# Optimization experiments

Measured on AMD Instinct MI355X. Metric: run time of the kernel, lower is better.

## Reference

```python
import jax, jax.numpy as jnp
import numpy as np

S = 14            # grid size, hardcoded via torch.arange(14) in the original
N = S * S         # 196 cells (one box per cell in this implementation)
B = 1024
NUM_CLS = 90
LAMBDA_COORD = 5.0
LAMBDA_NOOBJ = 0.5


def setup_inputs() -> dict:
    key = jax.random.key(0)
    k1, k2, k3 = jax.random.split(key, 3)
    p_yolo = jax.random.uniform(k1, (B, S, S, 5 + NUM_CLS), dtype=jnp.float32)
    g_yolo = jax.random.uniform(k2, (B, S, S, 5 + NUM_CLS), dtype=jnp.float32)
    obj = jax.random.uniform(k3, (B, S, S)) < 0.05
    g_yolo = g_yolo.at[..., 4].set(jnp.where(obj, g_yolo[..., 4], 0.0))
    return {"p_yolo": p_yolo, "g_yolo": g_yolo}


def reference(p_yolo, g_yolo):
    Bc = p_yolo.shape[0]
    dt = p_yolo.dtype
    # which cells contain an object (coo_mask), flattened row-major like torch
    valid = (g_yolo[..., 4] > 0).reshape(Bc, N)          # [B, N] bool
    vf = valid.astype(dt)
    pred = p_yolo[..., :5].reshape(Bc, N, 5)             # [B, N, 5]
    targ = g_yolo[..., :5].reshape(Bc, N, 5)             # [B, N, 5]

    # grid cell coordinates (row-major flatten matches torch boolean-mask order)
    rows = jnp.repeat(jnp.arange(S, dtype=dt), S)        # [N]
    cols = jnp.tile(jnp.arange(S, dtype=dt), S)          # [N]
    # cal_iou converts target xy to global coords IN PLACE before the xy mse
    tx = cols / S + targ[..., 0] / S                     # [B, N]
    ty = rows / S + targ[..., 1] / S
    tw, th = targ[..., 2], targ[..., 3]

    # IoU [B, Npred, Ntarg] -- same math as cal_iou (pred stays in local coords)
    dx = jnp.abs(tx[:, None, :] - pred[:, :, None, 0])
    dy = jnp.abs(ty[:, None, :] - pred[:, :, None, 1])
    sw = (tw[:, None, :] + pred[:, :, None, 2]) * 0.5
    sh = (th[:, None, :] + pred[:, :, None, 3]) * 0.5
    inter = jnp.maximum((sw - dx) * (sh - dy), 0.0)      # clamp after product, as original
    union = (tw * th)[:, None, :] + (pred[..., 2] * pred[..., 3])[:, :, None] - inter
    iou = inter / union

    # per-target best prediction (max over pred dim = dim 0 in original)
    best_iou = iou.max(axis=1)                           # [B, N]
    best_idx = iou.argmax(axis=1)                        # [B, N] int
    bp = jnp.take_along_axis(pred, best_idx[..., None], axis=1)  # [B, N, 5]

    # localization (xy) loss: matched pred xy vs global target xy, sum over valid targets
    xy_loss = jnp.sum(vf * ((bp[..., 0] - tx) ** 2 + (bp[..., 1] - ty) ** 2))

    # confidence loss for matched boxes: (pred_conf * iou - 1)^2
    con_obj_loss = jnp.sum(vf * (bp[..., 4] * best_iou - 1.0) ** 2)

    # no-object confidence loss: preds NOT selected by any valid target,
    # only counted for images that contain at least one object (original skips empty images)
    hit = jnp.zeros((Bc, N), dtype=dt).at[jnp.arange(Bc)[:, None], best_idx].max(vf)
    has_obj = vf.max(axis=1)                             # [B]
    nocon_obj_loss = jnp.sum(has_obj[:, None] * (1.0 - hit) * pred[..., 4] ** 2)

    # class loss over object cells (batched over all images)
    cls_d = (p_yolo[..., 5:] - g_yolo[..., 5:]).reshape(Bc, N, NUM_CLS)
    con_class_loss = jnp.sum(vf[..., None] * cls_d ** 2)

    # NOTE: original total doubles xy_loss and never uses wh_loss -- kept faithful
    total = (LAMBDA_COORD * (xy_loss + xy_loss) + con_obj_loss
             + LAMBDA_NOOBJ * nocon_obj_loss + con_class_loss) / Bc
    return total
```

## Files before the change

kernel.cpp:

```cpp
#include <hip/hip_runtime.h>
#include <math.h>

#define GS 14
#define NCELL 196
#define NCLS 90
#define CH 95

__global__ __launch_bounds__(256) void yolo_loss_main(
    const float* __restrict__ p, const float* __restrict__ g,
    float* __restrict__ ws, int B)
{
    int b = blockIdx.x;
    if (b >= B) return;
    const float* pb = p + (size_t)b * NCELL * CH;
    const float* gb = g + (size_t)b * NCELL * CH;

    __shared__ float sp[NCELL][5];
    __shared__ float st[NCELL][5];
    __shared__ int   svalid[NCELL];
    __shared__ int   scount;
    __shared__ int   shit[NCELL];
    __shared__ float sred[4];

    const int tid  = threadIdx.x;
    const int wave = tid >> 6;
    const int lane = tid & 63;

    for (int i = tid; i < NCELL * 5; i += 256) {
        int c = i / 5, j = i - c * 5;
        sp[c][j] = pb[c * CH + j];
        st[c][j] = gb[c * CH + j];
    }
    for (int i = tid; i < NCELL; i += 256) shit[i] = 0;
    __syncthreads();

    if (tid == 0) {
        int cnt = 0;
        for (int c = 0; c < NCELL; ++c)
            if (st[c][4] > 0.0f) svalid[cnt++] = c;
        scount = cnt;
    }
    __syncthreads();
    const int count = scount;

    float xy_acc = 0.0f, con_acc = 0.0f;

    for (int vt = wave; vt < count; vt += 4) {
        const int t = svalid[vt];
        const float tx = __fadd_rn(__fdiv_rn((float)(t % GS), (float)GS),
                                   __fdiv_rn(st[t][0], (float)GS));
        const float ty = __fadd_rn(__fdiv_rn((float)(t / GS), (float)GS),
                                   __fdiv_rn(st[t][1], (float)GS));
        const float tw = st[t][2], th = st[t][3];
        const float twth = __fmul_rn(tw, th);

        float bi = -INFINITY;
        int   bidx = 0x7fffffff;
        for (int pp = lane; pp < NCELL; pp += 64) {
            const float px = sp[pp][0], py = sp[pp][1];
            const float pw = sp[pp][2], ph = sp[pp][3];
            const float dx = fabsf(__fsub_rn(tx, px));
            const float dy = fabsf(__fsub_rn(ty, py));
            const float sw = __fmul_rn(__fadd_rn(tw, pw), 0.5f);
            const float sh = __fmul_rn(__fadd_rn(th, ph), 0.5f);
            const float inter = fmaxf(__fmul_rn(__fsub_rn(sw, dx),
                                                __fsub_rn(sh, dy)), 0.0f);
            const float uni = __fsub_rn(__fadd_rn(twth, __fmul_rn(pw, ph)), inter);
            const float iou = __fdiv_rn(inter, uni);
            if (iou > bi || (iou == bi && pp < bidx)) { bi = iou; bidx = pp; }
        }
        for (int off = 32; off; off >>= 1) {
            const float oi  = __shfl_xor(bi, off);
            const int   oid = __shfl_xor(bidx, off);
            if (oi > bi || (oi == bi && oid < bidx)) { bi = oi; bidx = oid; }
        }
        if (lane == 0) {
            const float d0 = __fsub_rn(sp[bidx][0], tx);
            const float d1 = __fsub_rn(sp[bidx][1], ty);
            xy_acc += __fadd_rn(__fmul_rn(d0, d0), __fmul_rn(d1, d1));
            const float cc = __fsub_rn(__fmul_rn(sp[bidx][4], bi), 1.0f);
            con_acc += __fmul_rn(cc, cc);
            shit[bidx] = 1;
        }
    }
    __syncthreads();

    float nocon_acc = 0.0f;
    if (count > 0) {
        for (int pp = tid; pp < NCELL; pp += 256) {
            if (!shit[pp]) {
                const float c = sp[pp][4];
                nocon_acc += c * c;
            }
        }
    }

    float cls_acc = 0.0f;
    const int totalc = count * NCLS;
    for (int i = tid; i < totalc; i += 256) {
        const int vt = i / NCLS, j = i - vt * NCLS;
        const int t = svalid[vt];
        const float d = pb[t * CH + 5 + j] - gb[t * CH + 5 + j];
        cls_acc += d * d;
    }

    float tot = 10.0f * xy_acc + con_acc + 0.5f * nocon_acc + cls_acc;
    for (int off = 32; off; off >>= 1) tot += __shfl_xor(tot, off);
    if (lane == 0) sred[wave] = tot;
    __syncthreads();
    if (tid == 0) ws[b] = sred[0] + sred[1] + sred[2] + sred[3];
}

__global__ __launch_bounds__(256) void yolo_loss_reduce(
    const float* __restrict__ ws, float* __restrict__ out, int B)
{
    const int tid = threadIdx.x;
    float s = 0.0f;
    for (int i = tid; i < B; i += 256) s += ws[i];
    for (int off = 32; off; off >>= 1) s += __shfl_xor(s, off);
    __shared__ float sr[4];
    if ((tid & 63) == 0) sr[tid >> 6] = s;
    __syncthreads();
    if (tid == 0) out[0] = (sr[0] + sr[1] + sr[2] + sr[3]) / (float)B;
}

extern "C" void kernel_launch(void* const* d_in, const int* in_sizes, int n_in,
                              void* d_out, int out_size, void* d_ws, size_t ws_size,
                              hipStream_t stream) {
    const float* p = (const float*)d_in[0];
    const float* g = (const float*)d_in[1];
    float* out = (float*)d_out;
    float* ws  = (float*)d_ws;
    const int B = in_sizes[0] / (NCELL * CH);

    yolo_loss_main<<<B, 256, 0, stream>>>(p, g, ws, B);
    yolo_loss_reduce<<<1, 256, 0, stream>>>(ws, out, B);
}
```

Measured before the change: 36.41 us.

## Fuse per-image loss and final reduction via atomicAdd; ballot-based valid-cell compaction

Replaces the serial single-thread scan that built the valid-target list with a wave ballot plus popcount prefix, so each of the 196 cells is checked and compacted in parallel. The head loads become one thread per cell. The separate reduction kernel is removed: each block atomically adds its scaled partial sum to the output, which is zeroed by a memset beforehand. This cuts one kernel launch and a serial bottleneck, but makes the float summation order nondeterministic.

```diff
diff --git a/kernel.cpp b/kernel.cpp
--- a/kernel.cpp
+++ b/kernel.cpp
@@ -6,19 +6,18 @@
 #define NCLS 90
 #define CH 95
 
-__global__ __launch_bounds__(256) void yolo_loss_main(
+__global__ __launch_bounds__(256) void yolo_loss_fused(
     const float* __restrict__ p, const float* __restrict__ g,
-    float* __restrict__ ws, int B)
+    float* __restrict__ out, float inv_b)
 {
-    int b = blockIdx.x;
-    if (b >= B) return;
+    const int b = blockIdx.x;
     const float* pb = p + (size_t)b * NCELL * CH;
     const float* gb = g + (size_t)b * NCELL * CH;
 
     __shared__ float sp[NCELL][5];
     __shared__ float st[NCELL][5];
     __shared__ int   svalid[NCELL];
-    __shared__ int   scount;
+    __shared__ unsigned long long smask[4];
     __shared__ int   shit[NCELL];
     __shared__ float sred[4];
 
@@ -26,22 +25,32 @@
     const int wave = tid >> 6;
     const int lane = tid & 63;
 
-    for (int i = tid; i < NCELL * 5; i += 256) {
-        int c = i / 5, j = i - c * 5;
-        sp[c][j] = pb[c * CH + j];
-        st[c][j] = gb[c * CH + j];
+    bool v = false;
+    if (tid < NCELL) {
+        const float* pr = pb + tid * CH;
+        const float* gr = gb + tid * CH;
+        float g4 = gr[4];
+        #pragma unroll
+        for (int j = 0; j < 4; ++j) { sp[tid][j] = pr[j]; st[tid][j] = gr[j]; }
+        sp[tid][4] = pr[4];
+        st[tid][4] = g4;
+        shit[tid] = 0;
+        v = g4 > 0.0f;
     }
-    for (int i = tid; i < NCELL; i += 256) shit[i] = 0;
+    const unsigned long long m = __ballot(v);
+    if (lane == 0) smask[wave] = m;
     __syncthreads();
 
-    if (tid == 0) {
-        int cnt = 0;
-        for (int c = 0; c < NCELL; ++c)
-            if (st[c][4] > 0.0f) svalid[cnt++] = c;
-        scount = cnt;
+    int base = 0;
+    #pragma unroll
+    for (int w = 0; w < 4; ++w) if (w < wave) base += __popcll(smask[w]);
+    const int count = __popcll(smask[0]) + __popcll(smask[1]) +
+                      __popcll(smask[2]) + __popcll(smask[3]);
+    if (v) {
+        const int pos = base + __popcll(m & ((1ull << lane) - 1ull));
+        svalid[pos] = tid;
     }
     __syncthreads();
-    const int count = scount;
 
     float xy_acc = 0.0f, con_acc = 0.0f;
 
@@ -86,12 +95,10 @@
     __syncthreads();
 
     float nocon_acc = 0.0f;
-    if (count > 0) {
-        for (int pp = tid; pp < NCELL; pp += 256) {
-            if (!shit[pp]) {
-                const float c = sp[pp][4];
-                nocon_acc += c * c;
-            }
+    if (count > 0 && tid < NCELL) {
+        if (!shit[tid]) {
+            const float c = sp[tid][4];
+            nocon_acc = c * c;
         }
     }
 
@@ -108,20 +115,10 @@
     for (int off = 32; off; off >>= 1) tot += __shfl_xor(tot, off);
     if (lane == 0) sred[wave] = tot;
     __syncthreads();
-    if (tid == 0) ws[b] = sred[0] + sred[1] + sred[2] + sred[3];
-}
-
-__global__ __launch_bounds__(256) void yolo_loss_reduce(
-    const float* __restrict__ ws, float* __restrict__ out, int B)
-{
-    const int tid = threadIdx.x;
-    float s = 0.0f;
-    for (int i = tid; i < B; i += 256) s += ws[i];
-    for (int off = 32; off; off >>= 1) s += __shfl_xor(s, off);
-    __shared__ float sr[4];
-    if ((tid & 63) == 0) sr[tid >> 6] = s;
-    __syncthreads();
-    if (tid == 0) out[0] = (sr[0] + sr[1] + sr[2] + sr[3]) / (float)B;
+    if (tid == 0) {
+        const float bl = sred[0] + sred[1] + sred[2] + sred[3];
+        atomicAdd(out, bl * inv_b);
+    }
 }
 
 extern "C" void kernel_launch(void* const* d_in, const int* in_sizes, int n_in,
@@ -130,9 +127,8 @@
     const float* p = (const float*)d_in[0];
     const float* g = (const float*)d_in[1];
     float* out = (float*)d_out;
-    float* ws  = (float*)d_ws;
     const int B = in_sizes[0] / (NCELL * CH);
 
-    yolo_loss_main<<<B, 256, 0, stream>>>(p, g, ws, B);
-    yolo_loss_reduce<<<1, 256, 0, stream>>>(ws, out, B);
+    hipMemsetAsync(out, 0, sizeof(float), stream);
+    yolo_loss_fused<<<B, 256, 0, stream>>>(p, g, out, 1.0f / (float)B);
 }
```

New measurement: 32.44 us, median of 2. 1.12x faster.
